# Kernel tuning notes

Hardware: AMD Instinct MI355X
Metric: run time of the kernel (lower is better)

The kernel has to match this reference:

```python
import jax, jax.numpy as jnp
import numpy as np

GROUP_SIZE = 128
ZERO_POINT = 8  # 4-bit symmetric zero point


def setup_inputs() -> dict:
    key = jax.random.key(0)
    k1, k2, k3, k4, k5, k6 = jax.random.split(key, 6)
    B, S, IN, OUT, RANK = 4, 2048, 4096, 4096, 32
    n_groups = IN // GROUP_SIZE  # 32
    x = jax.random.normal(k1, (B, S, IN), dtype=jnp.float32)
    q = jax.random.randint(k2, (OUT, IN), 0, 16, dtype=jnp.int32)  # 4-bit codes
    scales = jax.random.uniform(k3, (OUT, n_groups), dtype=jnp.float32)
    U = jax.random.normal(k4, (OUT, RANK), dtype=jnp.float32)
    V = jax.random.normal(k5, (RANK, IN), dtype=jnp.float32)
    bias = jax.random.normal(k6, (OUT,), dtype=jnp.float32)
    return {"x": x, "q": q, "scales": scales, "U": U, "V": V, "bias": bias}


def reference(x, q, scales, U, V, bias):
    out_f, in_f = q.shape
    n_groups = scales.shape[1]
    # Dequantize: per-group scaled 4-bit codes -> [out, in]
    qf = (q.astype(scales.dtype) - ZERO_POINT).reshape(out_f, n_groups, GROUP_SIZE)
    W = (qf * scales[:, :, None]).reshape(out_f, in_f)
    # Low-rank correction
    W = W + U @ V
    # F.linear: y = x @ W^T + b
    return jnp.einsum("bsi,oi->bso", x, W) + bias
```

## Files before the change

### kernel.cpp

```cpp
#include <hip/hip_runtime.h>
#include <hip/hip_bf16.h>

#define GAS __attribute__((address_space(1)))
#define LAS __attribute__((address_space(3)))

typedef __bf16 bf16x8 __attribute__((ext_vector_type(8)));
typedef float f32x16 __attribute__((ext_vector_type(16)));

constexpr int Kd = 4096;
constexpr int Nd = 4096;
constexpr int RANKd = 32;
constexpr int NG = 32;
constexpr int BM = 128, BN = 128, BK = 64;

constexpr int BWR = 32, BWC = 256;
constexpr int NBUILD = (Nd / BWR) * (Kd / BWC);

__global__ __launch_bounds__(256) void prep(
    const int* __restrict__ q, const float* __restrict__ scales,
    const float* __restrict__ U, const float* __restrict__ V,
    __hip_bfloat16* __restrict__ W,
    const float* __restrict__ x, __hip_bfloat16* __restrict__ xb)
{
  __shared__ float V_s[RANKd][BWC + 4];
  __shared__ float U_s[BWR][RANKd + 1];

  const int t = threadIdx.x;
  const int bid = blockIdx.x;

  if (bid >= NBUILD) {
    const size_t base = (size_t)(bid - NBUILD) * 8192;
    #pragma unroll
    for (int i = 0; i < 4; ++i) {
      const size_t idx = base + i * 2048 + t * 8;
      float4 a = *(const float4*)(x + idx);
      float4 b = *(const float4*)(x + idx + 4);
      union { __hip_bfloat16 h[8]; int4 v; } u;
      u.h[0] = __float2bfloat16(a.x); u.h[1] = __float2bfloat16(a.y);
      u.h[2] = __float2bfloat16(a.z); u.h[3] = __float2bfloat16(a.w);
      u.h[4] = __float2bfloat16(b.x); u.h[5] = __float2bfloat16(b.y);
      u.h[6] = __float2bfloat16(b.z); u.h[7] = __float2bfloat16(b.w);
      *(int4*)(xb + idx) = u.v;
    }
    return;
  }

  const int bx = bid & 15;
  const int by = bid >> 4;
  const int n0 = by * BWR;
  const int k0 = bx * BWC;

  {
    const int idx = t * 4;
    const int row = idx >> 5, rr = idx & 31;
    float4 uv = *(const float4*)(U + (size_t)(n0 + row) * RANKd + rr);
    U_s[row][rr] = uv.x; U_s[row][rr + 1] = uv.y;
    U_s[row][rr + 2] = uv.z; U_s[row][rr + 3] = uv.w;
  }
  #pragma unroll
  for (int i = 0; i < 8; ++i) {
    const int idx = i * 1024 + t * 4;
    const int vr = idx >> 8, vc = idx & 255;
    *(float4*)&V_s[vr][vc] = *(const float4*)(V + (size_t)vr * Kd + k0 + vc);
  }
  __syncthreads();

  const int rs = t >> 5;
  const int cs = t & 31;
  const int row0 = n0 + rs * 4;
  const int c0 = cs * 4;
  const int c1 = 128 + cs * 4;
  const int g0 = k0 >> 7, g1 = g0 + 1;

  float acc[4][8];
  #pragma unroll
  for (int j = 0; j < 4; ++j) {
    const int* qr = q + (size_t)(row0 + j) * Kd + k0;
    int4 a = *(const int4*)(qr + c0);
    int4 b = *(const int4*)(qr + c1);
    const float s0 = scales[(size_t)(row0 + j) * NG + g0];
    const float s1 = scales[(size_t)(row0 + j) * NG + g1];
    acc[j][0] = (float)(a.x - 8) * s0; acc[j][1] = (float)(a.y - 8) * s0;
    acc[j][2] = (float)(a.z - 8) * s0; acc[j][3] = (float)(a.w - 8) * s0;
    acc[j][4] = (float)(b.x - 8) * s1; acc[j][5] = (float)(b.y - 8) * s1;
    acc[j][6] = (float)(b.z - 8) * s1; acc[j][7] = (float)(b.w - 8) * s1;
  }

  #pragma unroll 4
  for (int r = 0; r < RANKd; ++r) {
    float4 v0 = *(const float4*)&V_s[r][c0];
    float4 v1 = *(const float4*)&V_s[r][c1];
    #pragma unroll
    for (int j = 0; j < 4; ++j) {
      const float u = U_s[rs * 4 + j][r];
      acc[j][0] += u * v0.x; acc[j][1] += u * v0.y;
      acc[j][2] += u * v0.z; acc[j][3] += u * v0.w;
      acc[j][4] += u * v1.x; acc[j][5] += u * v1.y;
      acc[j][6] += u * v1.z; acc[j][7] += u * v1.w;
    }
  }

  #pragma unroll
  for (int j = 0; j < 4; ++j) {
    union { __hip_bfloat16 h[4]; uint2 v; } o0, o1;
    o0.h[0] = __float2bfloat16(acc[j][0]); o0.h[1] = __float2bfloat16(acc[j][1]);
    o0.h[2] = __float2bfloat16(acc[j][2]); o0.h[3] = __float2bfloat16(acc[j][3]);
    o1.h[0] = __float2bfloat16(acc[j][4]); o1.h[1] = __float2bfloat16(acc[j][5]);
    o1.h[2] = __float2bfloat16(acc[j][6]); o1.h[3] = __float2bfloat16(acc[j][7]);
    __hip_bfloat16* wr = W + (size_t)(row0 + j) * Kd + k0;
    *(uint2*)(wr + c0) = o0.v;
    *(uint2*)(wr + c1) = o1.v;
  }
}

#define WAIT_VM4 asm volatile("s_waitcnt vmcnt(4)" ::: "memory")
#define WAIT_VM0 asm volatile("s_waitcnt vmcnt(0)" ::: "memory")

#define ISSUE4(G)                                                               \
  {                                                                             \
    const int so_ = ((G) & 1) * 16384;                                          \
    const size_t ko_ = (size_t)(G) * 32;                                        \
    __builtin_amdgcn_global_load_lds((GAS void*)(ag0 + ko_),                    \
        (LAS void*)(smc + so_ + ldsA), 16, 0, 0);                               \
    __builtin_amdgcn_global_load_lds((GAS void*)(ag1 + ko_),                    \
        (LAS void*)(smc + so_ + ldsA + 1024), 16, 0, 0);                        \
    __builtin_amdgcn_global_load_lds((GAS void*)(bg0 + ko_),                    \
        (LAS void*)(smc + so_ + ldsB), 16, 0, 0);                               \
    __builtin_amdgcn_global_load_lds((GAS void*)(bg1 + ko_),                    \
        (LAS void*)(smc + so_ + ldsB + 1024), 16, 0, 0);                        \
  }

#define GPHASE(G, WAITSTMT, DO_ISSUE)                                           \
  {                                                                             \
    WAITSTMT;                                                                   \
    __builtin_amdgcn_s_barrier();                                               \
    __builtin_amdgcn_sched_barrier(0);                                          \
    const char* as_ = (const char*)smc + ((G) & 1) * 16384;                     \
    bf16x8 af0[4], af1[4], bfA[2], bfB[2];                                      \
    _Pragma("unroll")                                                           \
    for (int mi = 0; mi < 4; ++mi) {                                            \
      af0[mi] = *(const bf16x8*)(as_ + aro + mi * 2048 + cq0);                  \
      af1[mi] = *(const bf16x8*)(as_ + aro + mi * 2048 + cq1);                  \
    }                                                                           \
    _Pragma("unroll")                                                           \
    for (int nj = 0; nj < 2; ++nj) {                                            \
      bfA[nj] = *(const bf16x8*)(as_ + bro + nj * 2048 + cq0);                  \
      bfB[nj] = *(const bf16x8*)(as_ + bro + nj * 2048 + cq1);                  \
    }                                                                           \
    asm volatile("s_waitcnt lgkmcnt(0)" ::: "memory");                          \
    __builtin_amdgcn_sched_barrier(0);                                          \
    __builtin_amdgcn_s_barrier();                                               \
    __builtin_amdgcn_sched_barrier(0);                                          \
    if (DO_ISSUE) { ISSUE4((G) + 2); }                                          \
    __builtin_amdgcn_sched_barrier(0);                                          \
    __builtin_amdgcn_s_setprio(1);                                              \
    _Pragma("unroll")                                                           \
    for (int mi = 0; mi < 4; ++mi)                                              \
      _Pragma("unroll")                                                         \
      for (int nj = 0; nj < 2; ++nj)                                            \
        acc[mi][nj] = __builtin_amdgcn_mfma_f32_32x32x16_bf16(                  \
            af0[mi], bfA[nj], acc[mi][nj], 0, 0, 0);                            \
    _Pragma("unroll")                                                           \
    for (int mi = 0; mi < 4; ++mi)                                              \
      _Pragma("unroll")                                                         \
      for (int nj = 0; nj < 2; ++nj)                                            \
        acc[mi][nj] = __builtin_amdgcn_mfma_f32_32x32x16_bf16(                  \
            af1[mi], bfB[nj], acc[mi][nj], 0, 0, 0);                            \
    __builtin_amdgcn_s_setprio(0);                                              \
  }

__global__ __launch_bounds__(512, 2) void gemm256(
    const __hip_bfloat16* __restrict__ A, const __hip_bfloat16* __restrict__ Bt,
    const float* __restrict__ bias, float* __restrict__ C)
{
  __shared__ __align__(16) char sm[65536];
  char* const smc = sm;

  int bx, by;
  {
    const int bid = blockIdx.x;
    if (gridDim.x == 512) {
      const int x = bid & 7, loc = bid >> 3;
      by = (x >> 2) * 16 + (loc & 15);
      bx = (x & 3) * 4 + (loc >> 4);
    } else {
      bx = bid % (Nd / 256);
      by = bid / (Nd / 256);
    }
  }
  const int bm0 = by * 256, bn0 = bx * 256;

  const int t = threadIdx.x;
  const int l = t & 63, w = t >> 6;

  const int sr   = l >> 2;
  const int schk = (l & 3) ^ ((l >> 3) & 3);
  const __hip_bfloat16* ag0 = A  + (size_t)(bm0 + w * 32 + sr) * Kd + schk * 8;
  const __hip_bfloat16* ag1 = ag0 + (size_t)16 * Kd;
  const __hip_bfloat16* bg0 = Bt + (size_t)(bn0 + w * 32 + sr) * Kd + schk * 8;
  const __hip_bfloat16* bg1 = bg0 + (size_t)16 * Kd;
  const int ldsA = w * 2048 + l * 16;
  const int ldsB = 32768 + ldsA;

  const int wm = w >> 2, wn = w & 3;
  const int rl = l & 31, kh = l >> 5, swz = (rl >> 1) & 3;
  const int aro = (wm * 128 + rl) * 64;
  const int bro = 32768 + (wn * 64 + rl) * 64;
  const int cq0 = (kh ^ swz) * 16;
  const int cq1 = ((2 + kh) ^ swz) * 16;

  f32x16 acc[4][2];
  #pragma unroll
  for (int mi = 0; mi < 4; ++mi)
    #pragma unroll
    for (int nj = 0; nj < 2; ++nj)
      acc[mi][nj] = (f32x16)(0.f);

  ISSUE4(0);
  ISSUE4(1);

  #pragma unroll 2
  for (int g = 0; g < 126; ++g) {
    GPHASE(g, WAIT_VM4, 1);
  }
  GPHASE(126, WAIT_VM4, 0);
  GPHASE(127, WAIT_VM0, 0);

  #pragma unroll
  for (int nj = 0; nj < 2; ++nj) {
    const int col = bn0 + wn * 64 + nj * 32 + rl;
    const float bz = bias[col];
    #pragma unroll
    for (int mi = 0; mi < 4; ++mi) {
      const int rbase = bm0 + wm * 128 + mi * 32 + 4 * kh;
      #pragma unroll
      for (int reg = 0; reg < 16; ++reg) {
        const int row = rbase + (reg & 3) + 8 * (reg >> 2);
        C[(size_t)row * Nd + col] = acc[mi][nj][reg] + bz;
      }
    }
  }
}

#undef GPHASE
#undef ISSUE4

template <bool ABF16>
__global__ __launch_bounds__(256) void gemm_bt(
    const void* __restrict__ Ap, const __hip_bfloat16* __restrict__ Bt,
    const float* __restrict__ bias, float* __restrict__ C)
{
  __shared__ __hip_bfloat16 As[BM * BK];
  __shared__ __hip_bfloat16 Bs[BN * BK];

  const int t  = threadIdx.x;
  const int l  = t & 63;
  const int w  = t >> 6;
  const int wm = w >> 1;
  const int wn = w & 1;
  const int bm0 = blockIdx.y * BM;
  const int bn0 = blockIdx.x * BN;

  f32x16 acc[2][2];
  #pragma unroll
  for (int i = 0; i < 2; ++i)
    #pragma unroll
    for (int j = 0; j < 2; ++j)
      acc[i][j] = (f32x16)(0.f);

  const __hip_bfloat16* Abf = (const __hip_bfloat16*)Ap;
  const float*          A32 = (const float*)Ap;

  const int sr   = l >> 2;
  const int schk = (l & 3) ^ ((l >> 3) & 3);
  const __hip_bfloat16* ag0 = Abf + (size_t)(bm0 + w * 32 + sr) * Kd + schk * 8;
  const __hip_bfloat16* bg0 = Bt  + (size_t)(bn0 + w * 32 + sr) * Kd + schk * 8;
  char* asb = (char*)As + w * 2048;
  char* bsb = (char*)Bs + w * 2048;

  const int rl = l & 31, kh = l >> 5, swz = (rl >> 1) & 3;
  const char* Ard = (const char*)As + (wm * 64 + rl) * 64;
  const char* Brd = (const char*)Bs + (wn * 64 + rl) * 64;

  const int arow = t >> 1, aslab = t & 1, arx = (arow >> 1) & 3;
  const float* a32p = A32 + (size_t)(bm0 + arow) * Kd + aslab * 32;
  char* awr = (char*)As + aslab * 8192 + arow * 64;

  for (int kt = 0; kt < Kd / BK; ++kt) {
    if constexpr (ABF16) {
      const __hip_bfloat16* ag = ag0 + kt * BK;
      __builtin_amdgcn_global_load_lds((GAS void*)ag,               (LAS void*)asb,                16, 0, 0);
      __builtin_amdgcn_global_load_lds((GAS void*)(ag + 16 * Kd),   (LAS void*)(asb + 1024),       16, 0, 0);
      __builtin_amdgcn_global_load_lds((GAS void*)(ag + 32),        (LAS void*)(asb + 8192),       16, 0, 0);
      __builtin_amdgcn_global_load_lds((GAS void*)(ag + 16*Kd + 32),(LAS void*)(asb + 8192 + 1024),16, 0, 0);
    } else {
      const float* ap = a32p + kt * BK;
      #pragma unroll
      for (int cc = 0; cc < 4; ++cc) {
        float4 f0 = ((const float4*)ap)[cc * 2];
        float4 f1 = ((const float4*)ap)[cc * 2 + 1];
        union { __hip_bfloat16 h[8]; int4 v; } u;
        u.h[0] = __float2bfloat16(f0.x); u.h[1] = __float2bfloat16(f0.y);
        u.h[2] = __float2bfloat16(f0.z); u.h[3] = __float2bfloat16(f0.w);
        u.h[4] = __float2bfloat16(f1.x); u.h[5] = __float2bfloat16(f1.y);
        u.h[6] = __float2bfloat16(f1.z); u.h[7] = __float2bfloat16(f1.w);
        *(int4*)(awr + ((cc ^ arx) * 16)) = u.v;
      }
    }
    {
      const __hip_bfloat16* bg = bg0 + kt * BK;
      __builtin_amdgcn_global_load_lds((GAS void*)bg,               (LAS void*)bsb,                16, 0, 0);
      __builtin_amdgcn_global_load_lds((GAS void*)(bg + 16 * Kd),   (LAS void*)(bsb + 1024),       16, 0, 0);
      __builtin_amdgcn_global_load_lds((GAS void*)(bg + 32),        (LAS void*)(bsb + 8192),       16, 0, 0);
      __builtin_amdgcn_global_load_lds((GAS void*)(bg + 16*Kd + 32),(LAS void*)(bsb + 8192 + 1024),16, 0, 0);
    }

    __syncthreads();

    bf16x8 af[2][4], bfr[2][4];
    #pragma unroll
    for (int mi = 0; mi < 2; ++mi)
      #pragma unroll
      for (int ks = 0; ks < 4; ++ks)
        af[mi][ks] = *(const bf16x8*)(Ard + (ks >> 1) * 8192 + mi * 2048 +
                                      ((((ks & 1) * 2 + kh) ^ swz) * 16));
    #pragma unroll
    for (int nj = 0; nj < 2; ++nj)
      #pragma unroll
      for (int ks = 0; ks < 4; ++ks)
        bfr[nj][ks] = *(const bf16x8*)(Brd + (ks >> 1) * 8192 + nj * 2048 +
                                       ((((ks & 1) * 2 + kh) ^ swz) * 16));

    #pragma unroll
    for (int ks = 0; ks < 4; ++ks)
      #pragma unroll
      for (int mi = 0; mi < 2; ++mi)
        #pragma unroll
        for (int nj = 0; nj < 2; ++nj)
          acc[mi][nj] = __builtin_amdgcn_mfma_f32_32x32x16_bf16(
              af[mi][ks], bfr[nj][ks], acc[mi][nj], 0, 0, 0);

    __syncthreads();
  }

  #pragma unroll
  for (int nj = 0; nj < 2; ++nj) {
    const int col = bn0 + wn * 64 + nj * 32 + rl;
    const float bz = bias[col];
    #pragma unroll
    for (int mi = 0; mi < 2; ++mi) {
      const int rbase = bm0 + wm * 64 + mi * 32 + 4 * kh;
      #pragma unroll
      for (int reg = 0; reg < 16; ++reg) {
        const int row = rbase + (reg & 3) + 8 * (reg >> 2);
        C[(size_t)row * Nd + col] = acc[mi][nj][reg] + bz;
      }
    }
  }
}

extern "C" void kernel_launch(void* const* d_in, const int* in_sizes, int n_in,
                              void* d_out, int out_size, void* d_ws, size_t ws_size,
                              hipStream_t stream)
{
  const float* x      = (const float*)d_in[0];
  const int*   q      = (const int*)  d_in[1];
  const float* scales = (const float*)d_in[2];
  const float* U      = (const float*)d_in[3];
  const float* V      = (const float*)d_in[4];
  const float* bias   = (const float*)d_in[5];
  float* out = (float*)d_out;

  const int M = in_sizes[0] / Kd;

  __hip_bfloat16* Wb = (__hip_bfloat16*)d_ws;
  const size_t wbytes = (size_t)Nd * Kd * sizeof(__hip_bfloat16);
  const size_t xbytes = (size_t)M  * Kd * sizeof(__hip_bfloat16);

  if (ws_size >= wbytes + xbytes && (M % 256) == 0) {
    __hip_bfloat16* Xb = (__hip_bfloat16*)((char*)d_ws + wbytes);
    const int nconv = (int)(((size_t)M * Kd) / 8192);
    prep<<<dim3(NBUILD + nconv), dim3(256), 0, stream>>>(q, scales, U, V, Wb, x, Xb);
    const int nblk = (M / 256) * (Nd / 256);
    gemm256<<<dim3(nblk), dim3(512), 0, stream>>>(Xb, Wb, bias, out);
  } else {
    prep<<<dim3(NBUILD), dim3(256), 0, stream>>>(q, scales, U, V, Wb, x, nullptr);
    dim3 grid(Nd / BN, M / BM);
    gemm_bt<false><<<grid, dim3(256), 0, stream>>>((const void*)x, Wb, bias, out);
  }
}
```

Measured before the change: 610.7 us.

## Switch GEMM to 128x256 tiles with 4 waves and triple-buffered LDS pipeline

Replaces the 256x256 tile, 512-thread GEMM with a 128x256 tile using 256 threads and a three-slot LDS ring. Next-stage global-to-LDS loads are now issued right after the LDS fragment reads, ahead of the wait and barrier, so more loads are in flight. The block swizzle is adjusted for the 1024-block grid. The cost is less reuse per tile (more global traffic for B per output) and higher LDS use per block, which may limit occupancy at two blocks per CU.

```diff
diff --git a/kernel.cpp b/kernel.cpp
--- a/kernel.cpp
+++ b/kernel.cpp
@@ -113,29 +113,31 @@
   }
 }
 
-#define WAIT_VM4 asm volatile("s_waitcnt vmcnt(4)" ::: "memory")
+#define WAIT_VM6 asm volatile("s_waitcnt vmcnt(6)" ::: "memory")
 #define WAIT_VM0 asm volatile("s_waitcnt vmcnt(0)" ::: "memory")
-
-#define ISSUE4(G)                                                               \
+#define WAIT_NONE ((void)0)
+
+#define ISSUE6(H, SLOT)                                                         \
   {                                                                             \
-    const int so_ = ((G) & 1) * 16384;                                          \
-    const size_t ko_ = (size_t)(G) * 32;                                        \
+    char* sb_ = smc + (SLOT) * 24576;                                           \
+    const size_t ko_ = (size_t)(H) * 32;                                        \
     __builtin_amdgcn_global_load_lds((GAS void*)(ag0 + ko_),                    \
-        (LAS void*)(smc + so_ + ldsA), 16, 0, 0);                               \
-    __builtin_amdgcn_global_load_lds((GAS void*)(ag1 + ko_),                    \
-        (LAS void*)(smc + so_ + ldsA + 1024), 16, 0, 0);                        \
+        (LAS void*)(sb_ + ldsA), 16, 0, 0);                                     \
+    __builtin_amdgcn_global_load_lds((GAS void*)(ag0 + 16 * Kd + ko_),          \
+        (LAS void*)(sb_ + ldsA + 1024), 16, 0, 0);                              \
     __builtin_amdgcn_global_load_lds((GAS void*)(bg0 + ko_),                    \
-        (LAS void*)(smc + so_ + ldsB), 16, 0, 0);                               \
-    __builtin_amdgcn_global_load_lds((GAS void*)(bg1 + ko_),                    \
-        (LAS void*)(smc + so_ + ldsB + 1024), 16, 0, 0);                        \
-  }
-
-#define GPHASE(G, WAITSTMT, DO_ISSUE)                                           \
+        (LAS void*)(sb_ + ldsB), 16, 0, 0);                                     \
+    __builtin_amdgcn_global_load_lds((GAS void*)(bg0 + 16 * Kd + ko_),          \
+        (LAS void*)(sb_ + ldsB + 1024), 16, 0, 0);                              \
+    __builtin_amdgcn_global_load_lds((GAS void*)(bg0 + 32 * Kd + ko_),          \
+        (LAS void*)(sb_ + ldsB + 2048), 16, 0, 0);                              \
+    __builtin_amdgcn_global_load_lds((GAS void*)(bg0 + 48 * Kd + ko_),          \
+        (LAS void*)(sb_ + ldsB + 3072), 16, 0, 0);                              \
+  }
+
+#define GPHASE(G, SCUR, SNXT2, WAITSTMT, DO_ISSUE)                              \
   {                                                                             \
-    WAITSTMT;                                                                   \
-    __builtin_amdgcn_s_barrier();                                               \
-    __builtin_amdgcn_sched_barrier(0);                                          \
-    const char* as_ = (const char*)smc + ((G) & 1) * 16384;                     \
+    const char* as_ = (const char*)smc + (SCUR) * 24576;                        \
     bf16x8 af0[4], af1[4], bfA[2], bfB[2];                                      \
     _Pragma("unroll")                                                           \
     for (int mi = 0; mi < 4; ++mi) {                                            \
@@ -147,11 +149,12 @@
       bfA[nj] = *(const bf16x8*)(as_ + bro + nj * 2048 + cq0);                  \
       bfB[nj] = *(const bf16x8*)(as_ + bro + nj * 2048 + cq1);                  \
     }                                                                           \
+    __builtin_amdgcn_sched_barrier(0);                                          \
+    if (DO_ISSUE) { ISSUE6((G) + 2, SNXT2); }                                   \
+    __builtin_amdgcn_sched_barrier(0);                                          \
+    WAITSTMT;                                                                   \
+    __builtin_amdgcn_s_barrier();                                               \
     asm volatile("s_waitcnt lgkmcnt(0)" ::: "memory");                          \
-    __builtin_amdgcn_sched_barrier(0);                                          \
-    __builtin_amdgcn_s_barrier();                                               \
-    __builtin_amdgcn_sched_barrier(0);                                          \
-    if (DO_ISSUE) { ISSUE4((G) + 2); }                                          \
     __builtin_amdgcn_sched_barrier(0);                                          \
     __builtin_amdgcn_s_setprio(1);                                              \
     _Pragma("unroll")                                                           \
@@ -167,28 +170,29 @@
         acc[mi][nj] = __builtin_amdgcn_mfma_f32_32x32x16_bf16(                  \
             af1[mi], bfB[nj], acc[mi][nj], 0, 0, 0);                            \
     __builtin_amdgcn_s_setprio(0);                                              \
-  }
-
-__global__ __launch_bounds__(512, 2) void gemm256(
+    __builtin_amdgcn_s_barrier();                                               \
+  }
+
+__global__ __launch_bounds__(256, 2) void gemm128(
     const __hip_bfloat16* __restrict__ A, const __hip_bfloat16* __restrict__ Bt,
     const float* __restrict__ bias, float* __restrict__ C)
 {
-  __shared__ __align__(16) char sm[65536];
+  __shared__ __align__(16) char sm[73728];
   char* const smc = sm;
 
   int bx, by;
   {
     const int bid = blockIdx.x;
-    if (gridDim.x == 512) {
+    if (gridDim.x == 1024) {
       const int x = bid & 7, loc = bid >> 3;
-      by = (x >> 2) * 16 + (loc & 15);
-      bx = (x & 3) * 4 + (loc >> 4);
+      by = x * 8 + (loc & 7);
+      bx = loc >> 3;
     } else {
-      bx = bid % (Nd / 256);
-      by = bid / (Nd / 256);
-    }
-  }
-  const int bm0 = by * 256, bn0 = bx * 256;
+      by = bid >> 4;
+      bx = bid & 15;
+    }
+  }
+  const int bm0 = by * 128, bn0 = bx * 256;
 
   const int t = threadIdx.x;
   const int l = t & 63, w = t >> 6;
@@ -196,16 +200,13 @@
   const int sr   = l >> 2;
   const int schk = (l & 3) ^ ((l >> 3) & 3);
   const __hip_bfloat16* ag0 = A  + (size_t)(bm0 + w * 32 + sr) * Kd + schk * 8;
-  const __hip_bfloat16* ag1 = ag0 + (size_t)16 * Kd;
-  const __hip_bfloat16* bg0 = Bt + (size_t)(bn0 + w * 32 + sr) * Kd + schk * 8;
-  const __hip_bfloat16* bg1 = bg0 + (size_t)16 * Kd;
+  const __hip_bfloat16* bg0 = Bt + (size_t)(bn0 + w * 64 + sr) * Kd + schk * 8;
   const int ldsA = w * 2048 + l * 16;
-  const int ldsB = 32768 + ldsA;
-
-  const int wm = w >> 2, wn = w & 3;
+  const int ldsB = 8192 + w * 4096 + l * 16;
+
   const int rl = l & 31, kh = l >> 5, swz = (rl >> 1) & 3;
-  const int aro = (wm * 128 + rl) * 64;
-  const int bro = 32768 + (wn * 64 + rl) * 64;
+  const int aro = rl * 64;
+  const int bro = 8192 + (w * 64 + rl) * 64;
   const int cq0 = (kh ^ swz) * 16;
   const int cq1 = ((2 + kh) ^ swz) * 16;
 
@@ -216,23 +217,27 @@
     for (int nj = 0; nj < 2; ++nj)
       acc[mi][nj] = (f32x16)(0.f);
 
-  ISSUE4(0);
-  ISSUE4(1);
-
-  #pragma unroll 2
-  for (int g = 0; g < 126; ++g) {
-    GPHASE(g, WAIT_VM4, 1);
-  }
-  GPHASE(126, WAIT_VM4, 0);
-  GPHASE(127, WAIT_VM0, 0);
+  ISSUE6(0, 0);
+  ISSUE6(1, 1);
+  WAIT_VM6;
+  __builtin_amdgcn_s_barrier();
+  __builtin_amdgcn_sched_barrier(0);
+
+  for (int g = 0; g < 126; g += 3) {
+    GPHASE(g,     0, 2, WAIT_VM6, 1);
+    GPHASE(g + 1, 1, 0, WAIT_VM6, 1);
+    GPHASE(g + 2, 2, 1, WAIT_VM6, 1);
+  }
+  GPHASE(126, 0, 2, WAIT_VM0, 0);
+  GPHASE(127, 1, 0, WAIT_NONE, 0);
 
   #pragma unroll
   for (int nj = 0; nj < 2; ++nj) {
-    const int col = bn0 + wn * 64 + nj * 32 + rl;
+    const int col = bn0 + w * 64 + nj * 32 + rl;
     const float bz = bias[col];
     #pragma unroll
     for (int mi = 0; mi < 4; ++mi) {
-      const int rbase = bm0 + wm * 128 + mi * 32 + 4 * kh;
+      const int rbase = bm0 + mi * 32 + 4 * kh;
       #pragma unroll
       for (int reg = 0; reg < 16; ++reg) {
         const int row = rbase + (reg & 3) + 8 * (reg >> 2);
@@ -243,7 +248,7 @@
 }
 
 #undef GPHASE
-#undef ISSUE4
+#undef ISSUE6
 
 template <bool ABF16>
 __global__ __launch_bounds__(256) void gemm_bt(
@@ -377,12 +382,12 @@
   const size_t wbytes = (size_t)Nd * Kd * sizeof(__hip_bfloat16);
   const size_t xbytes = (size_t)M  * Kd * sizeof(__hip_bfloat16);
 
-  if (ws_size >= wbytes + xbytes && (M % 256) == 0) {
+  if (ws_size >= wbytes + xbytes && (M % 128) == 0) {
     __hip_bfloat16* Xb = (__hip_bfloat16*)((char*)d_ws + wbytes);
     const int nconv = (int)(((size_t)M * Kd) / 8192);
     prep<<<dim3(NBUILD + nconv), dim3(256), 0, stream>>>(q, scales, U, V, Wb, x, Xb);
-    const int nblk = (M / 256) * (Nd / 256);
-    gemm256<<<dim3(nblk), dim3(512), 0, stream>>>(Xb, Wb, bias, out);
+    const int nblk = (M / 128) * (Nd / 256);
+    gemm128<<<dim3(nblk), dim3(256), 0, stream>>>(Xb, Wb, bias, out);
   } else {
     prep<<<dim3(NBUILD), dim3(256), 0, stream>>>(q, scales, U, V, Wb, x, nullptr);
     dim3 grid(Nd / BN, M / BM);
```

After: 551.9 us. -9.6%, faster.
